# Kernel tuning notes

Measured on AMD Instinct MI355X. Metric: run time of the kernel, lower is better.

## Reference

```python
import jax, jax.numpy as jnp
import numpy as np

D1 = 4096
D2 = 4096
K = 838860  # int(D1*D2*0.05)
ALPHA = 16.0


def setup_inputs() -> dict:
    key = jax.random.key(0)
    k1, k2, k3, k4, k5 = jax.random.split(key, 5)
    x = jax.random.normal(k1, (2, 64, D1), jnp.float32)
    W_base = jax.random.normal(k2, (D2, D1), jnp.float32) * 0.02  # torch Linear weight (out, in)
    b_base = jnp.zeros((D2,), jnp.float32)
    c_re = jax.random.normal(k3, (K,), jnp.float32) * 0.02
    c_im = jax.random.normal(k4, (K,), jnp.float32) * 0.02
    # unique flat positions of the top-k frequency coefficients (stand-in for topk of |fft2(delta_W_init)|)
    mask_idx = jax.random.permutation(k5, D1 * D2)[:K].astype(jnp.int32)
    return {"x": x, "W_base": W_base, "b_base": b_base,
            "c_re": c_re, "c_im": c_im, "mask_idx": mask_idx}


def reference(x, W_base, b_base, c_re, c_im, mask_idx):
    # scatter sparse complex coefficients into dense frequency matrix
    c = (c_re + 1j * c_im).astype(jnp.complex64)
    F_flat = jnp.zeros((D1 * D2,), jnp.complex64).at[mask_idx].set(c)
    # inverse 2D FFT -> real part -> scale by alpha
    Delta_W = jnp.fft.ifft2(F_flat.reshape(D1, D2)).real.astype(jnp.float32) * ALPHA  # [D1, D2]
    # frozen base linear: h = x @ W_base.T + b
    h = jnp.einsum('bnd,fd->bnf', x, W_base) + b_base
    # LoRA-style low-frequency update
    return h + jnp.einsum('bnd,df->bnf', x, Delta_W)
```

## Files before the change

### kernel.cpp

```cpp
#include <hip/hip_runtime.h>


#define TWO_PI 6.28318530717958647692f
constexpr int NROW = 128;
constexpr float SCALE_A = 16.0f / 16777216.0f;
constexpr int NCHUNK = 256;
constexpr int KC = 4;

typedef unsigned short ushort_t;
using short8 = __attribute__((ext_vector_type(8))) short;
using f32x4  = __attribute__((ext_vector_type(4))) float;

__device__ __forceinline__ ushort_t f2bf(float f) {
  unsigned u = __float_as_uint(f);
  u = (u + 0x7FFFu + ((u >> 16) & 1u)) >> 16;
  return (ushort_t)u;
}
__device__ __forceinline__ unsigned cvtpk(float lo, float hi) {
  unsigned r;
  asm("v_cvt_pk_bf16_f32 %0, %1, %2" : "=v"(r) : "v"(lo), "v"(hi));
  return r;
}
__device__ __forceinline__ float bflo(unsigned u) { return __int_as_float((int)(u << 16)); }
__device__ __forceinline__ float bfhi(unsigned u) { return __int_as_float((int)(u & 0xffff0000u)); }
__device__ __forceinline__ void dot2(float& acc, unsigned a, unsigned b) {
  asm("v_dot2_f32_bf16 %0, %1, %2, %0" : "+v"(acc) : "v"(a), "v"(b));
}
__device__ __forceinline__ void gload_lds16(const void* g, void* l) {
  __builtin_amdgcn_global_load_lds(
      (const __attribute__((address_space(1))) unsigned*)g,
      (__attribute__((address_space(3))) unsigned*)l, 16, 0, 0);
}

__global__ __launch_bounds__(1024) void fused_stage1(const float* __restrict__ x,
                                                     unsigned* __restrict__ XTb,
                                                     const int* __restrict__ idx, int K,
                                                     int chunk, int* __restrict__ cnt,
                                                     ushort_t* __restrict__ xbf) {
  __shared__ __align__(16) char smem[25600];
  const int bx = blockIdx.x, tid = threadIdx.x;
  if (bx >= 512) {
    int i = (bx - 512) * 1024 + tid;
    float4 v = ((const float4*)x)[i];
    ((uint2*)xbf)[i] = make_uint2(cvtpk(v.x, v.y), cvtpk(v.z, v.w));
    return;
  }
  if (bx < 256) {
    float*    xs   = (float*)smem;
    unsigned* bp   = (unsigned*)(smem + 16384);
    float2*   w64f = (float2*)(smem + 24576);
    unsigned* wA   = (unsigned*)(smem + 25088);
    unsigned* wB   = (unsigned*)(smem + 25344);
    const int t = bx & 127, qi = bx >> 7;
    const float* xrow = x + (size_t)t * 4096;
#pragma unroll
    for (int l = 0; l < 4; ++l) xs[tid + 1024 * l] = xrow[tid + 1024 * l];
    if (tid < 64) {
      float s, c; __sincosf(TWO_PI * (float)tid * (1.0f / 64.0f), &s, &c);
      w64f[tid] = make_float2(c, s);
      wA[tid] = cvtpk(c, -s);
      wB[tid] = cvtpk(s, c);
    }
    __syncthreads();
#pragma unroll
    for (int l = 0; l < 2; ++l) {
      int o = tid + 1024 * l, m1 = o >> 5, k1l = o & 31, k1 = qi * 32 + k1l;
      float ar = 0.f, ai = 0.f;
      for (int m2 = 0; m2 < 64; ++m2) {
        float xv = xs[m1 + (m2 << 6)];
        float2 w = w64f[(m2 * k1) & 63];
        ar = fmaf(xv, w.x, ar); ai = fmaf(xv, w.y, ai);
      }
      float s, c; __sincosf((float)(m1 * k1) * (TWO_PI / 4096.0f), &s, &c);
      bp[(m1 << 5) + k1l] = cvtpk(ar * c - ai * s, ar * s + ai * c);
    }
    __syncthreads();
    {
      const int k1l = tid & 31, k2 = tid >> 5;
      const int k = qi * 32 + k1l + (k2 << 6);
      float xr = 0.f, xi = 0.f;
      for (int m1 = 0; m1 < 64; ++m1) {
        unsigned wi = (unsigned)((m1 * k2) & 63);
        unsigned bv = bp[(m1 << 5) + k1l];
        dot2(xr, wA[wi], bv);
        dot2(xi, wB[wi], bv);
      }
      XTb[(size_t)k * NROW + t] = cvtpk(xr, xi);
      if (qi == 0 && tid == 0) {
        float xr2 = 0.f, xi2 = 0.f;
        for (int m1 = 0; m1 < 64; ++m1) {
          float sgn = (m1 & 1) ? -1.f : 1.f;
          unsigned bv = bp[m1 << 5];
          xr2 = fmaf(sgn, bflo(bv), xr2);
          xi2 = fmaf(sgn, bfhi(bv), xi2);
        }
        XTb[(size_t)2048 * NROW + t] = cvtpk(xr2, xi2);
      }
    }
  } else {
    int* h = (int*)smem;
    const int c = bx - 256;
#pragma unroll
    for (int l = 0; l < 4; ++l) h[tid + 1024 * l] = 0;
    __syncthreads();
    const int j0 = c * chunk, j1 = min(j0 + chunk, K);
    for (int j = j0 + tid; j < j1; j += 1024) atomicAdd(&h[idx[j] & 4095], 1);
    __syncthreads();
#pragma unroll
    for (int l = 0; l < 4; ++l) cnt[(size_t)c * 4096 + tid + 1024 * l] = h[tid + 1024 * l];
  }
}

__global__ __launch_bounds__(256) void colscan(int* __restrict__ cnt, int* __restrict__ tot) {
  const int k2 = blockIdx.x * 256 + threadIdx.x;
  int run = 0;
  for (int c8 = 0; c8 < NCHUNK; c8 += 8) {
    int v[8];
#pragma unroll
    for (int i = 0; i < 8; ++i) v[i] = cnt[(size_t)(c8 + i) * 4096 + k2];
#pragma unroll
    for (int i = 0; i < 8; ++i) {
      cnt[(size_t)(c8 + i) * 4096 + k2] = run;
      run += v[i];
    }
  }
  tot[k2] = run;
}

__global__ __launch_bounds__(1024) void scan4096(const int* __restrict__ count,
                                                 int* __restrict__ off) {
  __shared__ int s[4096];
  int tid = threadIdx.x;
#pragma unroll
  for (int l = 0; l < 4; ++l) s[tid + 1024 * l] = count[tid + 1024 * l];
  __syncthreads();
  for (int d = 1; d < 4096; d <<= 1) {
    int v[4];
#pragma unroll
    for (int l = 0; l < 4; ++l) {
      int i = tid + 1024 * l;
      v[l] = s[i] + ((i >= d) ? s[i - d] : 0);
    }
    __syncthreads();
#pragma unroll
    for (int l = 0; l < 4; ++l) s[tid + 1024 * l] = v[l];
    __syncthreads();
  }
#pragma unroll
  for (int l = 0; l < 4; ++l) {
    int i = tid + 1024 * l;
    off[i] = s[i] - count[i];
  }
}

__global__ __launch_bounds__(1024) void scatter2(const int* __restrict__ idx,
                                                 const float* __restrict__ cre,
                                                 const float* __restrict__ cim, int K,
                                                 int chunk, const int* __restrict__ base,
                                                 const int* __restrict__ off,
                                                 uint2* __restrict__ bucket) {
  __shared__ int lbase[4096];
  __shared__ int lcur[4096];
  const int c = blockIdx.x, tid = threadIdx.x;
#pragma unroll
  for (int l = 0; l < 4; ++l) {
    int k2 = tid + 1024 * l;
    lbase[k2] = base[(size_t)c * 4096 + k2] + off[k2];
    lcur[k2] = 0;
  }
  __syncthreads();
  const int j0 = c * chunk, j1 = min(j0 + chunk, K);
  for (int j = j0 + tid; j < j1; j += 1024) {
    int p = idx[j];
    int k2 = p & 4095;
    int r = atomicAdd(&lcur[k2], 1);
    unsigned cr = f2bf(cre[j]), ci = f2bf(cim[j]);
    bucket[lbase[k2] + r] = make_uint2((unsigned)(p >> 12) | (cr << 16), ci << 16);
  }
}

__global__ __launch_bounds__(256, 4) void fused_heavy(const uint2* __restrict__ bucket,
                                                      const int* __restrict__ off,
                                                      const int* __restrict__ count,
                                                      const unsigned* __restrict__ XTb,
                                                      unsigned* __restrict__ Yp,
                                                      const ushort_t* __restrict__ xbf,
                                                      const float* __restrict__ W,
                                                      ushort_t* __restrict__ partb) {
  __shared__ __align__(16) char smem[32768];
  const int tid = threadIdx.x;
  const int w = tid >> 6, lane = tid & 63;
  if (blockIdx.x >= 256) {
    float4* red = (float4*)smem;
    const int colsel = w >> 1, half = w & 1;
    const int k2 = (blockIdx.x - 256) * 2 + colsel;
    const int s = off[k2], n = count[k2];
    const unsigned voff = lane * 8;
    float ar0 = 0.f, ai0 = 0.f, ar1 = 0.f, ai1 = 0.f;
    for (int c = half * 64; c < n; c += 128) {
      int idx = c + lane;
      uint2 ec = (idx < n) ? bucket[s + idx] : make_uint2(0u, 0u);
#pragma unroll
      for (int g = 0; g < 64; g += 8) {
        unsigned Ap[8], Bp[8];
        uint2 xv0, xv1, xv2, xv3, xv4, xv5, xv6, xv7;
#pragma unroll
        for (int u = 0; u < 8; ++u) {
          unsigned w0 = (unsigned)__builtin_amdgcn_readlane((int)ec.x, g + u);
          unsigned w1 = (unsigned)__builtin_amdgcn_readlane((int)ec.y, g + u);
          int k1 = (int)(w0 & 0xfffu);
          unsigned cj = (k1 > 2048) ? 0x8000u : 0u;
          int r = (k1 > 2048) ? 4096 - k1 : k1;
          unsigned cr16 = w0 >> 16;
          unsigned ci16 = w1 >> 16;
          Ap[u] = cr16 | ((ci16 ^ 0x8000u ^ cj) << 16);
          Bp[u] = ci16 | ((cr16 ^ cj) << 16);
          const unsigned* p = XTb + (size_t)r * NROW;
          uint2* dst = (u == 0) ? &xv0 : (u == 1) ? &xv1 : (u == 2) ? &xv2 :
                       (u == 3) ? &xv3 : (u == 4) ? &xv4 : (u == 5) ? &xv5 :
                       (u == 6) ? &xv6 : &xv7;
          asm volatile("global_load_dwordx2 %0, %1, %2"
                       : "=v"(*dst) : "v"(voff), "s"(p) : "memory");
        }
        asm volatile("s_waitcnt vmcnt(0)"
                     : "+v"(xv0), "+v"(xv1), "+v"(xv2), "+v"(xv3),
                       "+v"(xv4), "+v"(xv5), "+v"(xv6), "+v"(xv7) :: "memory");
        __builtin_amdgcn_sched_barrier(0);
#pragma unroll
        for (int u = 0; u < 8; ++u) {
          uint2 xv = (u == 0) ? xv0 : (u == 1) ? xv1 : (u == 2) ? xv2 :
                     (u == 3) ? xv3 : (u == 4) ? xv4 : (u == 5) ? xv5 :
                     (u == 6) ? xv6 : xv7;
          dot2(ar0, Ap[u], xv.x);
          dot2(ai0, Bp[u], xv.x);
          dot2(ar1, Ap[u], xv.y);
          dot2(ai1, Bp[u], xv.y);
        }
      }
    }
    if (half == 1) red[colsel * 64 + lane] = make_float4(ar0, ai0, ar1, ai1);
    __syncthreads();
    if (half == 0) {
      float4 o = red[colsel * 64 + lane];
      ar0 += o.x; ai0 += o.y; ar1 += o.z; ai1 += o.w;
      Yp[(size_t)(2 * lane) * 4096 + k2]     = cvtpk(ar0, ai0);
      Yp[(size_t)(2 * lane + 1) * 4096 + k2] = cvtpk(ar1, ai1);
    }
  } else {
    ushort_t* xs = (ushort_t*)smem;
    float* wsf = (float*)(smem + 16384);
    const int f0 = (blockIdx.x & 63) * 64;
    const int kc = blockIdx.x >> 6;
    f32x4 acc[2][4];
#pragma unroll
    for (int i = 0; i < 2; ++i)
#pragma unroll
      for (int j = 0; j < 4; ++j) acc[i][j] = (f32x4){0.f, 0.f, 0.f, 0.f};
    const int kbeg = kc * 1024;
    for (int st = 0; st < 16; ++st) {
      const int k0 = kbeg + st * 64;
#pragma unroll
      for (int cc = 0; cc < 4; ++cc) {
        int lb = w * 4096 + cc * 1024;
        int e = (lb >> 1) + lane * 8;
        int r = e >> 6, sl = (e >> 3) & 7;
        gload_lds16(xbf + (size_t)r * 4096 + k0 + ((sl ^ (r & 7)) << 3),
                    (char*)xs + lb);
      }
#pragma unroll
      for (int cc = 0; cc < 4; ++cc) {
        int lb = w * 4096 + cc * 1024;
        int e32 = (lb >> 2) + lane * 4;
        int r = e32 >> 6, g = (e32 >> 2) & 15, s8 = g >> 1, h = g & 1;
        gload_lds16(W + (size_t)(f0 + r) * 4096 + k0 + ((s8 ^ (r & 7)) << 3) + (h << 2),
                    (char*)wsf + lb);
      }
      __syncthreads();
#pragma unroll
      for (int kk = 0; kk < 2; ++kk) {
        int ksA = kk * 4 + (lane >> 4);
        short8 af[2], bfr[4];
#pragma unroll
        for (int mf = 0; mf < 2; ++mf) {
          int ra = w * 32 + mf * 16 + (lane & 15);
          af[mf] = *(const short8*)(&xs[ra * 64 + ((ksA ^ (ra & 7)) << 3)]);
        }
#pragma unroll
        for (int nf = 0; nf < 4; ++nf) {
          int rb = nf * 16 + (lane & 15);
          const float* bpp = &wsf[rb * 64 + ((ksA ^ (rb & 7)) << 3)];
          float4 a4 = *(const float4*)bpp;
          float4 b4 = *(const float4*)(bpp + 4);
          union { uint4 u; short8 s; } pk;
          pk.u.x = cvtpk(a4.x, a4.y);
          pk.u.y = cvtpk(a4.z, a4.w);
          pk.u.z = cvtpk(b4.x, b4.y);
          pk.u.w = cvtpk(b4.z, b4.w);
          bfr[nf] = pk.s;
        }
#pragma unroll
        for (int mf = 0; mf < 2; ++mf)
#pragma unroll
          for (int nf = 0; nf < 4; ++nf)
            acc[mf][nf] = __builtin_amdgcn_mfma_f32_16x16x32_bf16(af[mf], bfr[nf], acc[mf][nf], 0, 0, 0);
      }
      __syncthreads();
    }
    ushort_t* pb = partb + ((size_t)kc << 19);
#pragma unroll
    for (int mf = 0; mf < 2; ++mf)
#pragma unroll
      for (int nf = 0; nf < 4; ++nf)
#pragma unroll
        for (int reg = 0; reg < 4; ++reg) {
          int row = w * 32 + mf * 16 + (lane >> 4) * 4 + reg;
          int col = f0 + nf * 16 + (lane & 15);
          pb[(size_t)row * 4096 + col] = f2bf(acc[mf][nf][reg]);
        }
  }
}

__global__ __launch_bounds__(1024) void dft_rows_y(const unsigned* __restrict__ Yp,
                                                   const ushort_t* __restrict__ partb,
                                                   const float* __restrict__ bias,
                                                   float* __restrict__ out) {
  __shared__ unsigned ys[4096];
  __shared__ unsigned bp[2048];
  __shared__ unsigned wA[64], wB[64];
  const int t = blockIdx.x, qi = blockIdx.y, tid = threadIdx.x;
  const unsigned* yrow = Yp + (size_t)t * 4096;
#pragma unroll
  for (int l = 0; l < 4; ++l) ys[tid + 1024 * l] = yrow[tid + 1024 * l];
  if (tid < 64) {
    float s, c; __sincosf(TWO_PI * (float)tid * (1.0f / 64.0f), &s, &c);
    wA[tid] = cvtpk(c, -s);
    wB[tid] = cvtpk(s, c);
  }
  __syncthreads();
#pragma unroll
  for (int l = 0; l < 2; ++l) {
    int o = tid + 1024 * l, a = o >> 5, n1l = o & 31, n1 = qi * 32 + n1l;
    float ar = 0.f, ai = 0.f;
    for (int b = 0; b < 64; ++b) {
      unsigned yv = ys[a + (b << 6)];
      unsigned wi = (unsigned)((n1 * b) & 63);
      dot2(ar, wA[wi], yv);
      dot2(ai, wB[wi], yv);
    }
    float s, c; __sincosf((float)(n1 * a) * (TWO_PI / 4096.0f), &s, &c);
    bp[(a << 5) + n1l] = cvtpk(ar * c - ai * s, ar * s + ai * c);
  }
  __syncthreads();
  float* orow = out + (size_t)t * 4096;
  const int n1l = tid & 31;
  const int n1 = qi * 32 + n1l;
#pragma unroll
  for (int l = 0; l < 2; ++l) {
    int n2 = (tid >> 5) + 32 * l;
    float accv = 0.f;
    for (int a = 0; a < 64; ++a)
      dot2(accv, wA[(unsigned)((n2 * a) & 63)], bp[(a << 5) + n1l]);
    int o = n1 + (n2 << 6);
    float sum = accv * SCALE_A + bias[o];
#pragma unroll
    for (int i = 0; i < KC; ++i)
      sum += bflo((unsigned)partb[((size_t)i << 19) + ((size_t)t << 12) + o] << 0) * 0.f +
             __int_as_float((int)((unsigned)partb[((size_t)i << 19) + ((size_t)t << 12) + o] << 16));
    orow[o] = sum;
  }
}

extern "C" void kernel_launch(void* const* d_in, const int* in_sizes, int n_in,
                              void* d_out, int out_size, void* d_ws, size_t ws_size,
                              hipStream_t stream) {
  const float* x   = (const float*)d_in[0];
  const float* W   = (const float*)d_in[1];
  const float* b   = (const float*)d_in[2];
  const float* cre = (const float*)d_in[3];
  const float* cim = (const float*)d_in[4];
  const int* midx  = (const int*)d_in[5];
  const int K = in_sizes[3];
  float* out = (float*)d_out;
  const int chunk = (K + NCHUNK - 1) / NCHUNK;

  char* ws = (char*)d_ws;
  unsigned* XTb   = (unsigned*)(ws);
  unsigned* Yp    = (unsigned*)(ws + ((size_t)2 << 20));
  ushort_t* xbf   = (ushort_t*)(ws + ((size_t)4 << 20));
  char* meta      = ws + ((size_t)5 << 20);
  int* tot = (int*)(meta);
  int* off = (int*)(meta + 16384);
  uint2* bucket   = (uint2*)(ws + ((size_t)5 << 20) + 262144);
  int* cnt        = (int*)(ws + ((size_t)12 << 20));
  ushort_t* partb = (ushort_t*)(ws + ((size_t)16 << 20));

  fused_stage1<<<640, 1024, 0, stream>>>(x, XTb, midx, K, chunk, cnt, xbf);
  colscan<<<16, 256, 0, stream>>>(cnt, tot);
  scan4096<<<1, 1024, 0, stream>>>(tot, off);
  scatter2<<<NCHUNK, 1024, 0, stream>>>(midx, cre, cim, K, chunk, cnt, off, bucket);
  fused_heavy<<<2304, 256, 0, stream>>>(bucket, off, tot, XTb, Yp, xbf, W, partb);
  dft_rows_y<<<dim3(NROW, 2), 1024, 0, stream>>>(Yp, partb, b, out);
}
```

Before: 111.5 us.

## Fuse scatter with dense GEMM and split sparse column DFT into its own kernel

```diff
diff --git a/kernel.cpp b/kernel.cpp
--- a/kernel.cpp
+++ b/kernel.cpp
@@ -153,104 +153,43 @@
   }
 }
 
-__global__ __launch_bounds__(1024) void scatter2(const int* __restrict__ idx,
-                                                 const float* __restrict__ cre,
-                                                 const float* __restrict__ cim, int K,
-                                                 int chunk, const int* __restrict__ base,
-                                                 const int* __restrict__ off,
-                                                 uint2* __restrict__ bucket) {
-  __shared__ int lbase[4096];
-  __shared__ int lcur[4096];
-  const int c = blockIdx.x, tid = threadIdx.x;
-#pragma unroll
-  for (int l = 0; l < 4; ++l) {
-    int k2 = tid + 1024 * l;
-    lbase[k2] = base[(size_t)c * 4096 + k2] + off[k2];
-    lcur[k2] = 0;
-  }
-  __syncthreads();
-  const int j0 = c * chunk, j1 = min(j0 + chunk, K);
-  for (int j = j0 + tid; j < j1; j += 1024) {
-    int p = idx[j];
-    int k2 = p & 4095;
-    int r = atomicAdd(&lcur[k2], 1);
-    unsigned cr = f2bf(cre[j]), ci = f2bf(cim[j]);
-    bucket[lbase[k2] + r] = make_uint2((unsigned)(p >> 12) | (cr << 16), ci << 16);
-  }
-}
-
-__global__ __launch_bounds__(256, 4) void fused_heavy(const uint2* __restrict__ bucket,
-                                                      const int* __restrict__ off,
-                                                      const int* __restrict__ count,
-                                                      const unsigned* __restrict__ XTb,
-                                                      unsigned* __restrict__ Yp,
-                                                      const ushort_t* __restrict__ xbf,
-                                                      const float* __restrict__ W,
-                                                      ushort_t* __restrict__ partb) {
+__global__ __launch_bounds__(256) void scatter_gemm(const int* __restrict__ idx,
+                                                    const float* __restrict__ cre,
+                                                    const float* __restrict__ cim, int K,
+                                                    int chunk, const int* __restrict__ base,
+                                                    const int* __restrict__ off,
+                                                    uint2* __restrict__ bucket,
+                                                    const ushort_t* __restrict__ xbf,
+                                                    const float* __restrict__ W,
+                                                    ushort_t* __restrict__ partb) {
   __shared__ __align__(16) char smem[32768];
   const int tid = threadIdx.x;
-  const int w = tid >> 6, lane = tid & 63;
-  if (blockIdx.x >= 256) {
-    float4* red = (float4*)smem;
-    const int colsel = w >> 1, half = w & 1;
-    const int k2 = (blockIdx.x - 256) * 2 + colsel;
-    const int s = off[k2], n = count[k2];
-    const unsigned voff = lane * 8;
-    float ar0 = 0.f, ai0 = 0.f, ar1 = 0.f, ai1 = 0.f;
-    for (int c = half * 64; c < n; c += 128) {
-      int idx = c + lane;
-      uint2 ec = (idx < n) ? bucket[s + idx] : make_uint2(0u, 0u);
-#pragma unroll
-      for (int g = 0; g < 64; g += 8) {
-        unsigned Ap[8], Bp[8];
-        uint2 xv0, xv1, xv2, xv3, xv4, xv5, xv6, xv7;
-#pragma unroll
-        for (int u = 0; u < 8; ++u) {
-          unsigned w0 = (unsigned)__builtin_amdgcn_readlane((int)ec.x, g + u);
-          unsigned w1 = (unsigned)__builtin_amdgcn_readlane((int)ec.y, g + u);
-          int k1 = (int)(w0 & 0xfffu);
-          unsigned cj = (k1 > 2048) ? 0x8000u : 0u;
-          int r = (k1 > 2048) ? 4096 - k1 : k1;
-          unsigned cr16 = w0 >> 16;
-          unsigned ci16 = w1 >> 16;
-          Ap[u] = cr16 | ((ci16 ^ 0x8000u ^ cj) << 16);
-          Bp[u] = ci16 | ((cr16 ^ cj) << 16);
-          const unsigned* p = XTb + (size_t)r * NROW;
-          uint2* dst = (u == 0) ? &xv0 : (u == 1) ? &xv1 : (u == 2) ? &xv2 :
-                       (u == 3) ? &xv3 : (u == 4) ? &xv4 : (u == 5) ? &xv5 :
-                       (u == 6) ? &xv6 : &xv7;
-          asm volatile("global_load_dwordx2 %0, %1, %2"
-                       : "=v"(*dst) : "v"(voff), "s"(p) : "memory");
-        }
-        asm volatile("s_waitcnt vmcnt(0)"
-                     : "+v"(xv0), "+v"(xv1), "+v"(xv2), "+v"(xv3),
-                       "+v"(xv4), "+v"(xv5), "+v"(xv6), "+v"(xv7) :: "memory");
-        __builtin_amdgcn_sched_barrier(0);
-#pragma unroll
-        for (int u = 0; u < 8; ++u) {
-          uint2 xv = (u == 0) ? xv0 : (u == 1) ? xv1 : (u == 2) ? xv2 :
-                     (u == 3) ? xv3 : (u == 4) ? xv4 : (u == 5) ? xv5 :
-                     (u == 6) ? xv6 : xv7;
-          dot2(ar0, Ap[u], xv.x);
-          dot2(ai0, Bp[u], xv.x);
-          dot2(ar1, Ap[u], xv.y);
-          dot2(ai1, Bp[u], xv.y);
-        }
-      }
-    }
-    if (half == 1) red[colsel * 64 + lane] = make_float4(ar0, ai0, ar1, ai1);
-    __syncthreads();
-    if (half == 0) {
-      float4 o = red[colsel * 64 + lane];
-      ar0 += o.x; ai0 += o.y; ar1 += o.z; ai1 += o.w;
-      Yp[(size_t)(2 * lane) * 4096 + k2]     = cvtpk(ar0, ai0);
-      Yp[(size_t)(2 * lane + 1) * 4096 + k2] = cvtpk(ar1, ai1);
+  if (blockIdx.x < 256) {
+    int* lbase = (int*)smem;
+    int* lcur  = (int*)(smem + 16384);
+    const int c = blockIdx.x;
+#pragma unroll
+    for (int l = 0; l < 16; ++l) {
+      int k2 = tid + 256 * l;
+      lbase[k2] = base[(size_t)c * 4096 + k2] + off[k2];
+      lcur[k2] = 0;
+    }
+    __syncthreads();
+    const int j0 = c * chunk, j1 = min(j0 + chunk, K);
+    for (int j = j0 + tid; j < j1; j += 256) {
+      int p = idx[j];
+      int k2 = p & 4095;
+      int r = atomicAdd(&lcur[k2], 1);
+      unsigned cr = f2bf(cre[j]), ci = f2bf(cim[j]);
+      bucket[lbase[k2] + r] = make_uint2((unsigned)(p >> 12) | (cr << 16), ci << 16);
     }
   } else {
     ushort_t* xs = (ushort_t*)smem;
     float* wsf = (float*)(smem + 16384);
-    const int f0 = (blockIdx.x & 63) * 64;
-    const int kc = blockIdx.x >> 6;
+    const int bg = blockIdx.x - 256;
+    const int f0 = (bg & 63) * 64;
+    const int kc = bg >> 6;
+    const int w = tid >> 6, lane = tid & 63;
     f32x4 acc[2][4];
 #pragma unroll
     for (int i = 0; i < 2; ++i)
@@ -320,6 +259,70 @@
   }
 }
 
+__global__ __launch_bounds__(256, 4) void spmm_col(const uint2* __restrict__ bucket,
+                                                   const int* __restrict__ off,
+                                                   const int* __restrict__ count,
+                                                   const unsigned* __restrict__ XTb,
+                                                   unsigned* __restrict__ Yp) {
+  __shared__ float4 red[2][64];
+  const int lane = threadIdx.x & 63;
+  const int wid = threadIdx.x >> 6;
+  const int colsel = wid >> 1, half = wid & 1;
+  const int k2 = blockIdx.x * 2 + colsel;
+  const int s = off[k2], n = count[k2];
+  const unsigned voff = lane * 8;
+  float ar0 = 0.f, ai0 = 0.f, ar1 = 0.f, ai1 = 0.f;
+  for (int c = half * 64; c < n; c += 128) {
+    int idx = c + lane;
+    uint2 ec = (idx < n) ? bucket[s + idx] : make_uint2(0u, 0u);
+#pragma unroll
+    for (int g = 0; g < 64; g += 8) {
+      unsigned Ap[8], Bp[8];
+      uint2 xv0, xv1, xv2, xv3, xv4, xv5, xv6, xv7;
+#pragma unroll
+      for (int u = 0; u < 8; ++u) {
+        unsigned w0 = (unsigned)__builtin_amdgcn_readlane((int)ec.x, g + u);
+        unsigned w1 = (unsigned)__builtin_amdgcn_readlane((int)ec.y, g + u);
+        int k1 = (int)(w0 & 0xfffu);
+        unsigned cj = (k1 > 2048) ? 0x8000u : 0u;
+        int r = (k1 > 2048) ? 4096 - k1 : k1;
+        unsigned cr16 = w0 >> 16;
+        unsigned ci16 = w1 >> 16;
+        Ap[u] = cr16 | ((ci16 ^ 0x8000u ^ cj) << 16);
+        Bp[u] = ci16 | ((cr16 ^ cj) << 16);
+        const unsigned* p = XTb + (size_t)r * NROW;
+        uint2* dst = (u == 0) ? &xv0 : (u == 1) ? &xv1 : (u == 2) ? &xv2 :
+                     (u == 3) ? &xv3 : (u == 4) ? &xv4 : (u == 5) ? &xv5 :
+                     (u == 6) ? &xv6 : &xv7;
+        asm volatile("global_load_dwordx2 %0, %1, %2"
+                     : "=v"(*dst) : "v"(voff), "s"(p) : "memory");
+      }
+      asm volatile("s_waitcnt vmcnt(0)"
+                   : "+v"(xv0), "+v"(xv1), "+v"(xv2), "+v"(xv3),
+                     "+v"(xv4), "+v"(xv5), "+v"(xv6), "+v"(xv7) :: "memory");
+      __builtin_amdgcn_sched_barrier(0);
+#pragma unroll
+      for (int u = 0; u < 8; ++u) {
+        uint2 xv = (u == 0) ? xv0 : (u == 1) ? xv1 : (u == 2) ? xv2 :
+                   (u == 3) ? xv3 : (u == 4) ? xv4 : (u == 5) ? xv5 :
+                   (u == 6) ? xv6 : xv7;
+        dot2(ar0, Ap[u], xv.x);
+        dot2(ai0, Bp[u], xv.x);
+        dot2(ar1, Ap[u], xv.y);
+        dot2(ai1, Bp[u], xv.y);
+      }
+    }
+  }
+  if (half == 1) red[colsel][lane] = make_float4(ar0, ai0, ar1, ai1);
+  __syncthreads();
+  if (half == 0) {
+    float4 o = red[colsel][lane];
+    ar0 += o.x; ai0 += o.y; ar1 += o.z; ai1 += o.w;
+    Yp[(size_t)(2 * lane) * 4096 + k2]     = cvtpk(ar0, ai0);
+    Yp[(size_t)(2 * lane + 1) * 4096 + k2] = cvtpk(ar1, ai1);
+  }
+}
+
 __global__ __launch_bounds__(1024) void dft_rows_y(const unsigned* __restrict__ Yp,
                                                    const ushort_t* __restrict__ partb,
                                                    const float* __restrict__ bias,
@@ -364,8 +367,7 @@
     float sum = accv * SCALE_A + bias[o];
 #pragma unroll
     for (int i = 0; i < KC; ++i)
-      sum += bflo((unsigned)partb[((size_t)i << 19) + ((size_t)t << 12) + o] << 0) * 0.f +
-             __int_as_float((int)((unsigned)partb[((size_t)i << 19) + ((size_t)t << 12) + o] << 16));
+      sum += __int_as_float((int)((unsigned)partb[((size_t)i << 19) + ((size_t)t << 12) + o] << 16));
     orow[o] = sum;
   }
 }
@@ -397,7 +399,8 @@
   fused_stage1<<<640, 1024, 0, stream>>>(x, XTb, midx, K, chunk, cnt, xbf);
   colscan<<<16, 256, 0, stream>>>(cnt, tot);
   scan4096<<<1, 1024, 0, stream>>>(tot, off);
-  scatter2<<<NCHUNK, 1024, 0, stream>>>(midx, cre, cim, K, chunk, cnt, off, bucket);
-  fused_heavy<<<2304, 256, 0, stream>>>(bucket, off, tot, XTb, Yp, xbf, W, partb);
+  scatter_gemm<<<512, 256, 0, stream>>>(midx, cre, cim, K, chunk, cnt, off, bucket,
+                                        xbf, W, partb);
+  spmm_col<<<2048, 256, 0, stream>>>(bucket, off, tot, XTb, Yp);
   dft_rows_y<<<dim3(NROW, 2), 1024, 0, stream>>>(Yp, partb, b, out);
 }
```

Measured after the change: 113.9 us. +2.1%, slower.
